# Performance work log

Hardware: AMD Instinct MI355X
Metric: run time of the kernel (lower is better)

## Reference

```python
import jax, jax.numpy as jnp
import numpy as np

B, P, E, H = 2, 4096, 512, 8
D = E // H
EPS = 1e-5


def _layernorm2d(x, g, b):
    # LayerNorm over last two dims (patches, embed) jointly, per torch nn.LayerNorm([P, E])
    mu = jnp.mean(x, axis=(-2, -1), keepdims=True)
    var = jnp.mean(jnp.square(x - mu), axis=(-2, -1), keepdims=True)
    return (x - mu) * jax.lax.rsqrt(var + EPS) * g + b


def setup_inputs() -> dict:
    key = jax.random.key(0)
    ks = jax.random.split(key, 4)
    s_in = 1.0 / np.sqrt(E)
    s_hid = 1.0 / np.sqrt(3 * E)
    return {
        "x": jax.random.normal(ks[0], (B, P, E), dtype=jnp.float32),
        "g1": jnp.ones((P, E), jnp.float32),
        "b1": jnp.zeros((P, E), jnp.float32),
        "W1": jax.random.normal(ks[1], (3 * E, E), jnp.float32) * s_in,
        "g2": jnp.ones((P, E), jnp.float32),
        "b2": jnp.zeros((P, E), jnp.float32),
        "Wa": jax.random.normal(ks[2], (3 * E, E), jnp.float32) * s_in,
        "ba": jnp.zeros((3 * E,), jnp.float32),
        "Wb": jax.random.normal(ks[3], (E, 3 * E), jnp.float32) * s_hid,
        "bb": jnp.zeros((E,), jnp.float32),
    }


def reference(x, g1, b1, W1, g2, b2, Wa, ba, Wb, bb):
    # --- attention branch ---
    h = _layernorm2d(x, g1, b1)                      # [B,P,E]
    qkv = h @ W1.T                                   # [B,P,3E]
    qkv = qkv.reshape(B, P, 3, H, D).transpose(2, 0, 3, 1, 4)  # [3,B,H,P,D]
    q, k, v = qkv[0], qkv[1], qkv[2]
    scale = 1.0 / jnp.sqrt(jnp.float32(D))
    dp = jnp.einsum("bhqd,bhkd->bhqk", q, k) * scale  # [B,H,P,P]
    # NOTE: softmax over axis -2 (the query axis), as in the original code
    dp = jax.nn.softmax(dp, axis=-2)
    wv = jnp.einsum("bhqk,bhkd->bhqd", dp, v)        # [B,H,P,D]
    wv = wv.transpose(0, 2, 1, 3).reshape(B, P, E)   # [B,P,E]
    out1 = x + wv
    # --- MLP branch ---
    h2 = _layernorm2d(out1, g2, b2)
    h2 = jax.nn.gelu(h2 @ Wa.T + ba, approximate=False)
    h2 = jax.nn.gelu(h2 @ Wb.T + bb, approximate=False)
    return h2 + out1
```

## Files before the change

### kernel.cpp

```cpp
#include <hip/hip_runtime.h>
#include <math.h>

typedef __bf16 bf16x8 __attribute__((ext_vector_type(8)));
typedef __bf16 bf16x4 __attribute__((ext_vector_type(4)));
typedef short s16x4 __attribute__((ext_vector_type(4)));
typedef float f32x4 __attribute__((ext_vector_type(4)));
typedef unsigned int u32x2 __attribute__((ext_vector_type(2)));
typedef unsigned short u16;
typedef unsigned int u32;

__device__ __forceinline__ void gl_lds16(const void* g, void* l) {
  __builtin_amdgcn_global_load_lds(
      (const __attribute__((address_space(1))) void*)g,
      (__attribute__((address_space(3))) void*)l, 16, 0, 0);
}

__device__ __forceinline__ u16 f2bf(float x) {
  union { float f; u32 u; } v; v.f = x;
  u32 r = v.u + 0x7FFFu + ((v.u >> 16) & 1u);
  return (u16)(r >> 16);
}

__device__ __forceinline__ u32 pack_bf2(float a, float b) {
  union { float f; u32 u; } ua, ub; ua.f = a; ub.f = b;
  return ((ua.u + 0x8000u) >> 16) | ((ub.u + 0x8000u) & 0xFFFF0000u);
}

__device__ __forceinline__ float expfast(float x) {
#if __has_builtin(__builtin_amdgcn_exp2f)
  return __builtin_amdgcn_exp2f(x);
#else
  return exp2f(x);
#endif
}

__device__ __forceinline__ f32x4 mfma16(bf16x4 a, bf16x4 b, f32x4 c) {
#if __has_builtin(__builtin_amdgcn_mfma_f32_16x16x16_bf16)
  return __builtin_amdgcn_mfma_f32_16x16x16_bf16(a, b, c, 0, 0, 0);
#else
  return __builtin_amdgcn_mfma_f32_16x16x16bf16_1k(
      __builtin_bit_cast(s16x4, a), __builtin_bit_cast(s16x4, b), c, 0, 0, 0);
#endif
}

__device__ __forceinline__ float gelu_f(float v) {
  return 0.5f * v * (1.0f + erff(v * 0.7071067811865475f));
}

__global__ void castbf3(const float* __restrict__ s0, const float* __restrict__ s1,
                        const float* __restrict__ s2, u16* __restrict__ d0,
                        u16* __restrict__ d1, u16* __restrict__ d2) {
  int blk = blockIdx.x;
  const float* s; u16* d;
  if (blk < 768)       { s = s0; d = d0; }
  else if (blk < 1536) { s = s1; d = d1; blk -= 768; }
  else                 { s = s2; d = d2; blk -= 1536; }
  int i = blk * 256 + threadIdx.x;
  float4 v = ((const float4*)s)[i];
  uint2 o;
  o.x = (u32)f2bf(v.x) | ((u32)f2bf(v.y) << 16);
  o.y = (u32)f2bf(v.z) | ((u32)f2bf(v.w) << 16);
  ((uint2*)d)[i] = o;
}

__global__ void ln_reduce(const float* __restrict__ src, float2* __restrict__ part) {
  int b = blockIdx.y;
  const float4* p = (const float4*)(src + (size_t)b * 2097152 + (size_t)blockIdx.x * 16384);
  float s = 0.f, q = 0.f;
  #pragma unroll
  for (int i = 0; i < 16; i++) {
    float4 v = p[i * 256 + threadIdx.x];
    s += v.x + v.y + v.z + v.w;
    q += v.x * v.x + v.y * v.y + v.z * v.z + v.w * v.w;
  }
  #pragma unroll
  for (int off = 32; off; off >>= 1) { s += __shfl_down(s, off, 64); q += __shfl_down(q, off, 64); }
  __shared__ float ls[4], lq[4];
  int w = threadIdx.x >> 6;
  if ((threadIdx.x & 63) == 0) { ls[w] = s; lq[w] = q; }
  __syncthreads();
  if (threadIdx.x == 0)
    part[b * 128 + blockIdx.x] =
        make_float2(ls[0] + ls[1] + ls[2] + ls[3], lq[0] + lq[1] + lq[2] + lq[3]);
}

__global__ void ln_final(const float2* __restrict__ part, float2* __restrict__ stats) {
  int b = blockIdx.x, t = threadIdx.x;
  float2 a = part[b * 128 + t], c = part[b * 128 + 64 + t];
  float s = a.x + c.x, q = a.y + c.y;
  #pragma unroll
  for (int off = 32; off; off >>= 1) { s += __shfl_down(s, off, 64); q += __shfl_down(q, off, 64); }
  if (t == 0) {
    const float inv = 1.0f / 2097152.0f;
    float mu = s * inv, var = q * inv - mu * mu;
    stats[b] = make_float2(mu, rsqrtf(var + 1e-5f));
  }
}

__global__ void ln_apply(const float* __restrict__ src, const float* __restrict__ g,
                         const float* __restrict__ bta, const float2* __restrict__ stats,
                         u16* __restrict__ dst) {
  int i = blockIdx.x * 256 + threadIdx.x;
  int b = i >= 524288;
  float2 st = stats[b];
  int r = i - b * 524288;
  float4 v = ((const float4*)src)[i];
  float4 gv = ((const float4*)g)[r];
  float4 bv = ((const float4*)bta)[r];
  float h0 = (v.x - st.x) * st.y * gv.x + bv.x;
  float h1 = (v.y - st.x) * st.y * gv.y + bv.y;
  float h2 = (v.z - st.x) * st.y * gv.z + bv.z;
  float h3 = (v.w - st.x) * st.y * gv.w + bv.w;
  uint2 o;
  o.x = (u32)f2bf(h0) | ((u32)f2bf(h1) << 16);
  o.y = (u32)f2bf(h2) | ((u32)f2bf(h3) << 16);
  ((uint2*)dst)[i] = o;
}

template <int MODE>
__global__ __launch_bounds__(256, 2)
void gemm_bt(const u16* __restrict__ A, const u16* __restrict__ Bm,
             const float* __restrict__ bias, const float* __restrict__ res,
             float* __restrict__ outf, u16* __restrict__ outb,
             int M, int N, int K) {
  __shared__ u16 As[128 * 32], Bs[128 * 32];
  const int tid = threadIdx.x;
  const int m0 = blockIdx.y * 128, n0 = blockIdx.x * 128;
  const int lane = tid & 63, w = tid >> 6;
  const int wm = (w >> 1) * 64, wn = (w & 1) * 64;
  const int c = lane & 15, quad = lane >> 4;
  const int arow = tid >> 2, acol = (tid & 3) * 8;

  const u16* gA = A + (size_t)(m0 + arow) * K + acol;
  const u16* gB = Bm + (size_t)(n0 + arow) * K + acol;
  u16* lA = As + tid * 8;
  u16* lB = Bs + tid * 8;

  f32x4 acc[4][4] = {};
  for (int kt = 0; kt < K; kt += 32) {
    gl_lds16(gA, lA);
    gl_lds16(gA + (size_t)64 * K, lA + 64 * 32);
    gl_lds16(gB, lB);
    gl_lds16(gB + (size_t)64 * K, lB + 64 * 32);
    gA += 32; gB += 32;
    __syncthreads();
    bf16x8 af[4], bf[4];
    #pragma unroll
    for (int i = 0; i < 4; i++) {
      af[i] = *(const bf16x8*)&As[(wm + i * 16 + c) * 32 + quad * 8];
      bf[i] = *(const bf16x8*)&Bs[(wn + i * 16 + c) * 32 + quad * 8];
    }
    #pragma unroll
    for (int i = 0; i < 4; i++)
      #pragma unroll
      for (int j = 0; j < 4; j++)
        acc[i][j] = __builtin_amdgcn_mfma_f32_16x16x32_bf16(af[i], bf[j], acc[i][j], 0, 0, 0);
    __syncthreads();
  }
  #pragma unroll
  for (int i = 0; i < 4; i++) {
    const int row0 = m0 + wm + i * 16 + quad * 4;
    #pragma unroll
    for (int j = 0; j < 4; j++) {
      const int col = n0 + wn + j * 16 + c;
      #pragma unroll
      for (int r = 0; r < 4; r++) {
        float v = acc[i][j][r];
        size_t oi = (size_t)(row0 + r) * N + col;
        if (MODE == 0 && col < 512) v *= 0.1803368801111204f;
        if (MODE == 1 || MODE == 2) v = gelu_f(v + bias[col]);
        if (MODE == 2) outf[oi] = v + res[oi];
        else           outb[oi] = f2bf(v);
      }
    }
  }
}

__global__ __launch_bounds__(256, 4)
void attn_pass1(const u16* __restrict__ qkv, float* __restrict__ rlpart) {
  __shared__ u16 Qs[2][2 * 128 * 32];
  const int tid = threadIdx.x;
  const int bh = blockIdx.y, b = bh >> 3, h = bh & 7;
  const int k0 = blockIdx.x * 128;
  const int lane = tid & 63, w = tid >> 6;
  const int wn = w * 32;
  const int c = lane & 15, quad = lane >> 4;
  const int arow = tid >> 2, acol = (tid & 3) * 8;

  bf16x8 bk[2][2];
  {
    const u16* Kg = qkv + ((size_t)(b * 4096 + k0 + wn + c)) * 1536 + 512 + h * 64 + quad * 8;
    #pragma unroll
    for (int j = 0; j < 2; j++)
      #pragma unroll
      for (int ks = 0; ks < 2; ks++)
        bk[j][ks] = *(const bf16x8*)(Kg + (size_t)j * 16 * 1536 + ks * 32);
  }
  const u16* Qg = qkv + ((size_t)(b * 4096 + blockIdx.z * 2048)) * 1536 + h * 64;

  #define STAGE_Q(t)                                                              \
    {                                                                             \
      u16* dst = Qs[(t) & 1];                                                     \
      const u16* src = Qg + (size_t)((t) * 128) * 1536;                           \
      _Pragma("unroll")                                                           \
      for (int ks = 0; ks < 2; ks++)                                              \
        _Pragma("unroll")                                                         \
        for (int rr = 0; rr < 128; rr += 64)                                      \
          gl_lds16(src + (size_t)(rr + arow) * 1536 + ks * 32 + acol,             \
                   dst + ks * 4096 + (rr + arow) * 32 + acol);                    \
    }

  STAGE_Q(0);
  float s0 = 0.f, s1 = 0.f;
  for (int t = 0; t < 16; t++) {
    __syncthreads();
    if (t + 1 < 16) STAGE_Q(t + 1);
    const u16* buf = Qs[t & 1];
    #pragma unroll
    for (int i = 0; i < 8; i++) {
      bf16x8 a0 = *(const bf16x8*)&buf[(i * 16 + c) * 32 + quad * 8];
      bf16x8 a1 = *(const bf16x8*)&buf[4096 + (i * 16 + c) * 32 + quad * 8];
      f32x4 acc0 = {}, acc1 = {};
      acc0 = __builtin_amdgcn_mfma_f32_16x16x32_bf16(a0, bk[0][0], acc0, 0, 0, 0);
      acc0 = __builtin_amdgcn_mfma_f32_16x16x32_bf16(a1, bk[0][1], acc0, 0, 0, 0);
      acc1 = __builtin_amdgcn_mfma_f32_16x16x32_bf16(a0, bk[1][0], acc1, 0, 0, 0);
      acc1 = __builtin_amdgcn_mfma_f32_16x16x32_bf16(a1, bk[1][1], acc1, 0, 0, 0);
      #pragma unroll
      for (int r = 0; r < 4; r++) {
        s0 += expfast(acc0[r]);
        s1 += expfast(acc1[r]);
      }
    }
  }
  #undef STAGE_Q
  s0 += __shfl_xor(s0, 16, 64); s0 += __shfl_xor(s0, 32, 64);
  s1 += __shfl_xor(s1, 16, 64); s1 += __shfl_xor(s1, 32, 64);
  if (quad == 0) {
    float* rp = rlpart + ((size_t)blockIdx.z * 16 + bh) * 4096 + k0 + wn;
    rp[c] = s0;
    rp[16 + c] = s1;
  }
}

__global__ void rl_comb(const float* __restrict__ part, float* __restrict__ rl) {
  int i = blockIdx.x * 256 + threadIdx.x;
  rl[i] = 1.0f / (part[i] + part[65536 + i]);
}

__global__ void vtrans(const u16* __restrict__ qkv, const float* __restrict__ rl,
                       u16* __restrict__ vt) {
  __shared__ u16 t[64 * 66];
  int bh = blockIdx.y, p0 = blockIdx.x * 64;
  int b = bh >> 3, h = bh & 7;
  const u16* src = qkv + ((size_t)(b * 4096 + p0)) * 1536 + 1024 + h * 64;
  const float* rp = rl + (size_t)bh * 4096 + p0;
  int tid = threadIdx.x;
  #pragma unroll
  for (int j = 0; j < 16; j++) {
    int idx = j * 256 + tid;
    int p = idx >> 6, d = idx & 63;
    union { float f; u32 u; } uv;
    uv.u = ((u32)src[(size_t)p * 1536 + d]) << 16;
    t[d * 66 + p] = f2bf(uv.f * rp[p]);
  }
  __syncthreads();
  u16* dst = vt + (size_t)bh * 262144 + (size_t)blockIdx.x * 4096;
  #pragma unroll
  for (int j = 0; j < 16; j++) {
    int idx = j * 256 + tid;
    int d = idx >> 6, p = idx & 63;
    dst[d * 64 + ((((p >> 3) & 7) ^ (d & 7)) << 3) + (p & 7)] = t[d * 66 + p];
  }
}

__global__ __launch_bounds__(256, 2)
void attn_pass2(const u16* __restrict__ qkv, const u16* __restrict__ vt,
                const float* __restrict__ x, float* __restrict__ out1) {
  __shared__ u16 Ks[2][2][2048];
  __shared__ u16 Vs[2][4096];
  const int tid = threadIdx.x;
  const int bh = blockIdx.y, b = bh >> 3, h = bh & 7;
  const int q0 = blockIdx.x * 128;
  const int lane = tid & 63, w = tid >> 6;
  const int wq = w * 32;
  const int c = lane & 15, quad = lane >> 4;

  bf16x8 bq[2][2];
  {
    const u16* Qg = qkv + ((size_t)(b * 4096 + q0 + wq + c)) * 1536 + h * 64 + quad * 8;
    #pragma unroll
    for (int j = 0; j < 2; j++)
      #pragma unroll
      for (int ks = 0; ks < 2; ks++)
        bq[j][ks] = *(const bf16x8*)(Qg + (size_t)j * 16 * 1536 + ks * 32);
  }
  const u16* Kg = qkv + ((size_t)b * 4096) * 1536 + 512 + h * 64;
  const u16* Vg = vt + (size_t)bh * 262144;

  #define STAGE_KV(t)                                                             \
    {                                                                             \
      const int buf_ = (t) & 1;                                                   \
      const int krow_ = (t) * 64 + (tid >> 2);                                    \
      _Pragma("unroll")                                                           \
      for (int ks = 0; ks < 2; ks++)                                              \
        gl_lds16(Kg + (size_t)krow_ * 1536 + ks * 32 + (tid & 3) * 8,             \
                 &Ks[buf_][ks][tid * 8]);                                         \
      gl_lds16(Vg + (t) * 4096 + tid * 8, &Vs[buf_][tid * 8]);                    \
      gl_lds16(Vg + (t) * 4096 + 2048 + tid * 8, &Vs[buf_][2048 + tid * 8]);      \
    }

  STAGE_KV(0);
  f32x4 oacc[2][4] = {};
  for (int t = 0; t < 64; t++) {
    __syncthreads();
    if (t + 1 < 64) STAGE_KV(t + 1);
    const int buf = t & 1;

    f32x4 sacc[4][2] = {};
    #pragma unroll
    for (int i = 0; i < 4; i++) {
      bf16x8 af0 = *(const bf16x8*)&Ks[buf][0][(i * 16 + c) * 32 + quad * 8];
      bf16x8 af1 = *(const bf16x8*)&Ks[buf][1][(i * 16 + c) * 32 + quad * 8];
      #pragma unroll
      for (int j = 0; j < 2; j++) {
        sacc[i][j] = __builtin_amdgcn_mfma_f32_16x16x32_bf16(af0, bq[j][0], sacc[i][j], 0, 0, 0);
        sacc[i][j] = __builtin_amdgcn_mfma_f32_16x16x32_bf16(af1, bq[j][1], sacc[i][j], 0, 0, 0);
      }
    }
    bf16x4 pa[4][2];
    #pragma unroll
    for (int i = 0; i < 4; i++)
      #pragma unroll
      for (int j = 0; j < 2; j++) {
        u32x2 pk;
        pk.x = pack_bf2(expfast(sacc[i][j][0]), expfast(sacc[i][j][1]));
        pk.y = pack_bf2(expfast(sacc[i][j][2]), expfast(sacc[i][j][3]));
        pa[i][j] = __builtin_bit_cast(bf16x4, pk);
      }
    #pragma unroll
    for (int kc = 0; kc < 4; kc++) {
      const int kb = 2 * kc + (quad >> 1);
      #pragma unroll
      for (int j2 = 0; j2 < 4; j2++) {
        const int d = j2 * 16 + c;
        bf16x4 vf = *(const bf16x4*)&Vs[buf][d * 64 + ((kb ^ (d & 7)) << 3) + 4 * (quad & 1)];
        oacc[0][j2] = mfma16(pa[kc][0], vf, oacc[0][j2]);
        oacc[1][j2] = mfma16(pa[kc][1], vf, oacc[1][j2]);
      }
    }
  }
  #undef STAGE_KV
  #pragma unroll
  for (int i2 = 0; i2 < 2; i2++)
    #pragma unroll
    for (int j2 = 0; j2 < 4; j2++)
      #pragma unroll
      for (int r = 0; r < 4; r++) {
        const int q = q0 + wq + i2 * 16 + quad * 4 + r;
        const int d = j2 * 16 + c;
        size_t oi = ((size_t)(b * 4096 + q)) * 512 + h * 64 + d;
        out1[oi] = x[oi] + oacc[i2][j2][r];
      }
}

extern "C" void kernel_launch(void* const* d_in, const int* in_sizes, int n_in,
                              void* d_out, int out_size, void* d_ws, size_t ws_size,
                              hipStream_t stream) {
  const float* x  = (const float*)d_in[0];
  const float* g1 = (const float*)d_in[1];
  const float* b1 = (const float*)d_in[2];
  const float* W1 = (const float*)d_in[3];
  const float* g2 = (const float*)d_in[4];
  const float* b2 = (const float*)d_in[5];
  const float* Wa = (const float*)d_in[6];
  const float* ba = (const float*)d_in[7];
  const float* Wb = (const float*)d_in[8];
  const float* bb = (const float*)d_in[9];
  float* out = (float*)d_out;

  char* ws = (char*)d_ws;
  u16* w1b   = (u16*)(ws);
  u16* wab   = (u16*)(ws + 1572864);
  u16* wbb   = (u16*)(ws + 3145728);
  u16* h1    = (u16*)(ws + 4718592);
  u16* qkv   = (u16*)(ws + 13107200);
  u16* vt    = (u16*)(ws + 38273024);
  u16* h2    = (u16*)(ws + 46661632);
  u16* mid   = (u16*)(ws + 55050240);
  float* rl  = (float*)(ws + 80216064);
  float* o1  = (float*)(ws + 80478208);
  float2* part  = (float2*)(ws + 97255424);
  float2* stats = (float2*)(ws + 97257472);
  float* rlpart = (float*)(ws + 55050240);

  castbf3<<<2304, 256, 0, stream>>>(W1, Wa, Wb, w1b, wab, wbb);

  ln_reduce<<<dim3(128, 2), 256, 0, stream>>>(x, part);
  ln_final<<<2, 64, 0, stream>>>(part, stats);
  ln_apply<<<4096, 256, 0, stream>>>(x, g1, b1, stats, h1);

  gemm_bt<0><<<dim3(12, 64), 256, 0, stream>>>(h1, w1b, nullptr, nullptr, nullptr, qkv,
                                               8192, 1536, 512);
  attn_pass1<<<dim3(32, 16, 2), 256, 0, stream>>>(qkv, rlpart);
  rl_comb<<<256, 256, 0, stream>>>(rlpart, rl);
  vtrans<<<dim3(64, 16), 256, 0, stream>>>(qkv, rl, vt);
  attn_pass2<<<dim3(32, 16), 256, 0, stream>>>(qkv, vt, x, o1);

  ln_reduce<<<dim3(128, 2), 256, 0, stream>>>(o1, part);
  ln_final<<<2, 64, 0, stream>>>(part, stats);
  ln_apply<<<4096, 256, 0, stream>>>(o1, g2, b2, stats, h2);

  gemm_bt<1><<<dim3(12, 64), 256, 0, stream>>>(h2, wab, ba, nullptr, nullptr, mid,
                                               8192, 1536, 512);
  gemm_bt<2><<<dim3(4, 64), 256, 0, stream>>>(mid, wbb, bb, o1, out, nullptr,
                                              8192, 512, 1536);
}
```

Before: 389.0 us.

## Fuse small launches and use 16x16x32 MFMA with LDS-staged probabilities in attention

Merges the weight casts with the first LayerNorm reduction into one launch. It also folds the LayerNorm finalization into each ln_apply block and the reciprocal-sum combine into vtrans, which removes four small kernel launches and their serialization. In attn_pass2, the exponentiated scores are written to a swizzled LDS buffer and read back as 8-wide fragments, so the PV product uses the 16x16x32 MFMA instead of 16x16x16. This trades extra LDS traffic and redundant per-block stat reductions for fewer launches and a denser MFMA instruction.

Result: faster. 367.3 us (-5.6%).

```diff
diff --git a/kernel.cpp b/kernel.cpp
--- a/kernel.cpp
+++ b/kernel.cpp
@@ -3,9 +3,7 @@
 
 typedef __bf16 bf16x8 __attribute__((ext_vector_type(8)));
 typedef __bf16 bf16x4 __attribute__((ext_vector_type(4)));
-typedef short s16x4 __attribute__((ext_vector_type(4)));
 typedef float f32x4 __attribute__((ext_vector_type(4)));
-typedef unsigned int u32x2 __attribute__((ext_vector_type(2)));
 typedef unsigned short u16;
 typedef unsigned int u32;
 
@@ -34,33 +32,47 @@
 #endif
 }
 
-__device__ __forceinline__ f32x4 mfma16(bf16x4 a, bf16x4 b, f32x4 c) {
-#if __has_builtin(__builtin_amdgcn_mfma_f32_16x16x16_bf16)
-  return __builtin_amdgcn_mfma_f32_16x16x16_bf16(a, b, c, 0, 0, 0);
-#else
-  return __builtin_amdgcn_mfma_f32_16x16x16bf16_1k(
-      __builtin_bit_cast(s16x4, a), __builtin_bit_cast(s16x4, b), c, 0, 0, 0);
-#endif
-}
-
 __device__ __forceinline__ float gelu_f(float v) {
   return 0.5f * v * (1.0f + erff(v * 0.7071067811865475f));
 }
 
-__global__ void castbf3(const float* __restrict__ s0, const float* __restrict__ s1,
-                        const float* __restrict__ s2, u16* __restrict__ d0,
-                        u16* __restrict__ d1, u16* __restrict__ d2) {
+__global__ void cast_lnred(const float* __restrict__ s0, const float* __restrict__ s1,
+                           const float* __restrict__ s2, u16* __restrict__ d0,
+                           u16* __restrict__ d1, u16* __restrict__ d2,
+                           const float* __restrict__ x, float2* __restrict__ part) {
   int blk = blockIdx.x;
-  const float* s; u16* d;
-  if (blk < 768)       { s = s0; d = d0; }
-  else if (blk < 1536) { s = s1; d = d1; blk -= 768; }
-  else                 { s = s2; d = d2; blk -= 1536; }
-  int i = blk * 256 + threadIdx.x;
-  float4 v = ((const float4*)s)[i];
-  uint2 o;
-  o.x = (u32)f2bf(v.x) | ((u32)f2bf(v.y) << 16);
-  o.y = (u32)f2bf(v.z) | ((u32)f2bf(v.w) << 16);
-  ((uint2*)d)[i] = o;
+  if (blk < 2304) {
+    const float* s; u16* d;
+    if (blk < 768)       { s = s0; d = d0; }
+    else if (blk < 1536) { s = s1; d = d1; blk -= 768; }
+    else                 { s = s2; d = d2; blk -= 1536; }
+    int i = blk * 256 + threadIdx.x;
+    float4 v = ((const float4*)s)[i];
+    uint2 o;
+    o.x = (u32)f2bf(v.x) | ((u32)f2bf(v.y) << 16);
+    o.y = (u32)f2bf(v.z) | ((u32)f2bf(v.w) << 16);
+    ((uint2*)d)[i] = o;
+    return;
+  }
+  blk -= 2304;
+  int b = blk >> 7, ib = blk & 127;
+  const float4* p = (const float4*)(x + (size_t)b * 2097152 + (size_t)ib * 16384);
+  float s = 0.f, q = 0.f;
+  #pragma unroll
+  for (int i = 0; i < 16; i++) {
+    float4 v = p[i * 256 + threadIdx.x];
+    s += v.x + v.y + v.z + v.w;
+    q += v.x * v.x + v.y * v.y + v.z * v.z + v.w * v.w;
+  }
+  #pragma unroll
+  for (int off = 32; off; off >>= 1) { s += __shfl_down(s, off, 64); q += __shfl_down(q, off, 64); }
+  __shared__ float ls[4], lq[4];
+  int w = threadIdx.x >> 6;
+  if ((threadIdx.x & 63) == 0) { ls[w] = s; lq[w] = q; }
+  __syncthreads();
+  if (threadIdx.x == 0)
+    part[b * 128 + ib] =
+        make_float2(ls[0] + ls[1] + ls[2] + ls[3], lq[0] + lq[1] + lq[2] + lq[3]);
 }
 
 __global__ void ln_reduce(const float* __restrict__ src, float2* __restrict__ part) {
@@ -84,33 +96,28 @@
         make_float2(ls[0] + ls[1] + ls[2] + ls[3], lq[0] + lq[1] + lq[2] + lq[3]);
 }
 
-__global__ void ln_final(const float2* __restrict__ part, float2* __restrict__ stats) {
-  int b = blockIdx.x, t = threadIdx.x;
-  float2 a = part[b * 128 + t], c = part[b * 128 + 64 + t];
-  float s = a.x + c.x, q = a.y + c.y;
-  #pragma unroll
-  for (int off = 32; off; off >>= 1) { s += __shfl_down(s, off, 64); q += __shfl_down(q, off, 64); }
-  if (t == 0) {
-    const float inv = 1.0f / 2097152.0f;
-    float mu = s * inv, var = q * inv - mu * mu;
-    stats[b] = make_float2(mu, rsqrtf(var + 1e-5f));
-  }
-}
-
 __global__ void ln_apply(const float* __restrict__ src, const float* __restrict__ g,
-                         const float* __restrict__ bta, const float2* __restrict__ stats,
+                         const float* __restrict__ bta, const float2* __restrict__ part,
                          u16* __restrict__ dst) {
   int i = blockIdx.x * 256 + threadIdx.x;
   int b = i >= 524288;
-  float2 st = stats[b];
+  int lane = threadIdx.x & 63;
+  float2 a = part[b * 128 + lane], c2 = part[b * 128 + 64 + lane];
+  float s = a.x + c2.x, q = a.y + c2.y;
+  #pragma unroll
+  for (int off = 32; off; off >>= 1) { s += __shfl_down(s, off, 64); q += __shfl_down(q, off, 64); }
+  s = __shfl(s, 0, 64); q = __shfl(q, 0, 64);
+  const float inv = 1.0f / 2097152.0f;
+  float mu = s * inv;
+  float rsig = rsqrtf(q * inv - mu * mu + 1e-5f);
   int r = i - b * 524288;
   float4 v = ((const float4*)src)[i];
   float4 gv = ((const float4*)g)[r];
   float4 bv = ((const float4*)bta)[r];
-  float h0 = (v.x - st.x) * st.y * gv.x + bv.x;
-  float h1 = (v.y - st.x) * st.y * gv.y + bv.y;
-  float h2 = (v.z - st.x) * st.y * gv.z + bv.z;
-  float h3 = (v.w - st.x) * st.y * gv.w + bv.w;
+  float h0 = (v.x - mu) * rsig * gv.x + bv.x;
+  float h1 = (v.y - mu) * rsig * gv.y + bv.y;
+  float h2 = (v.z - mu) * rsig * gv.z + bv.z;
+  float h3 = (v.w - mu) * rsig * gv.w + bv.w;
   uint2 o;
   o.x = (u32)f2bf(h0) | ((u32)f2bf(h1) << 16);
   o.y = (u32)f2bf(h2) | ((u32)f2bf(h3) << 16);
@@ -242,26 +249,26 @@
   }
 }
 
-__global__ void rl_comb(const float* __restrict__ part, float* __restrict__ rl) {
-  int i = blockIdx.x * 256 + threadIdx.x;
-  rl[i] = 1.0f / (part[i] + part[65536 + i]);
-}
-
-__global__ void vtrans(const u16* __restrict__ qkv, const float* __restrict__ rl,
+__global__ void vtrans(const u16* __restrict__ qkv, const float* __restrict__ rlpart,
                        u16* __restrict__ vt) {
   __shared__ u16 t[64 * 66];
+  __shared__ float rls[64];
   int bh = blockIdx.y, p0 = blockIdx.x * 64;
   int b = bh >> 3, h = bh & 7;
   const u16* src = qkv + ((size_t)(b * 4096 + p0)) * 1536 + 1024 + h * 64;
-  const float* rp = rl + (size_t)bh * 4096 + p0;
   int tid = threadIdx.x;
+  if (tid < 64) {
+    size_t idx = (size_t)bh * 4096 + p0 + tid;
+    rls[tid] = 1.0f / (rlpart[idx] + rlpart[65536 + idx]);
+  }
+  __syncthreads();
   #pragma unroll
   for (int j = 0; j < 16; j++) {
     int idx = j * 256 + tid;
     int p = idx >> 6, d = idx & 63;
     union { float f; u32 u; } uv;
     uv.u = ((u32)src[(size_t)p * 1536 + d]) << 16;
-    t[d * 66 + p] = f2bf(uv.f * rp[p]);
+    t[d * 66 + p] = f2bf(uv.f * rls[p]);
   }
   __syncthreads();
   u16* dst = vt + (size_t)bh * 262144 + (size_t)blockIdx.x * 4096;
@@ -278,6 +285,7 @@
                 const float* __restrict__ x, float* __restrict__ out1) {
   __shared__ u16 Ks[2][2][2048];
   __shared__ u16 Vs[2][4096];
+  __shared__ u16 Ps[128][64];
   const int tid = threadIdx.x;
   const int bh = blockIdx.y, b = bh >> 3, h = bh & 7;
   const int q0 = blockIdx.x * 128;
@@ -327,39 +335,52 @@
         sacc[i][j] = __builtin_amdgcn_mfma_f32_16x16x32_bf16(af1, bq[j][1], sacc[i][j], 0, 0, 0);
       }
     }
-    bf16x4 pa[4][2];
-    #pragma unroll
-    for (int i = 0; i < 4; i++)
+    #pragma unroll
+    for (int i = 0; i < 4; i++) {
+      const int blk = i * 2 + (quad >> 1);
       #pragma unroll
       for (int j = 0; j < 2; j++) {
-        u32x2 pk;
+        const int qloc = wq + j * 16 + c;
+        u16* pp = &Ps[qloc][((blk ^ (qloc & 7)) << 3) + ((quad & 1) << 2)];
+        uint2 pk;
         pk.x = pack_bf2(expfast(sacc[i][j][0]), expfast(sacc[i][j][1]));
         pk.y = pack_bf2(expfast(sacc[i][j][2]), expfast(sacc[i][j][3]));
-        pa[i][j] = __builtin_bit_cast(bf16x4, pk);
-      }
-    #pragma unroll
-    for (int kc = 0; kc < 4; kc++) {
-      const int kb = 2 * kc + (quad >> 1);
-      #pragma unroll
-      for (int j2 = 0; j2 < 4; j2++) {
-        const int d = j2 * 16 + c;
-        bf16x4 vf = *(const bf16x4*)&Vs[buf][d * 64 + ((kb ^ (d & 7)) << 3) + 4 * (quad & 1)];
-        oacc[0][j2] = mfma16(pa[kc][0], vf, oacc[0][j2]);
-        oacc[1][j2] = mfma16(pa[kc][1], vf, oacc[1][j2]);
-      }
+        *(uint2*)pp = pk;
+      }
+    }
+    #pragma unroll
+    for (int kg = 0; kg < 2; kg++) {
+      bf16x8 pf[2], vf[4];
+      #pragma unroll
+      for (int j = 0; j < 2; j++) {
+        const int qloc = wq + j * 16 + c;
+        const int blk = kg * 4 + quad;
+        pf[j] = *(const bf16x8*)&Ps[qloc][(blk ^ (qloc & 7)) << 3];
+      }
+      #pragma unroll
+      for (int dt = 0; dt < 4; dt++) {
+        const int d = dt * 16 + c;
+        const int vblk = kg * 4 + quad;
+        vf[dt] = *(const bf16x8*)&Vs[buf][d * 64 + ((vblk ^ (d & 7)) << 3)];
+      }
+      #pragma unroll
+      for (int j = 0; j < 2; j++)
+        #pragma unroll
+        for (int dt = 0; dt < 4; dt++)
+          oacc[j][dt] = __builtin_amdgcn_mfma_f32_16x16x32_bf16(pf[j], vf[dt], oacc[j][dt], 0, 0, 0);
     }
   }
   #undef STAGE_KV
   #pragma unroll
-  for (int i2 = 0; i2 < 2; i2++)
-    #pragma unroll
-    for (int j2 = 0; j2 < 4; j2++)
+  for (int j = 0; j < 2; j++)
+    #pragma unroll
+    for (int dt = 0; dt < 4; dt++)
       #pragma unroll
       for (int r = 0; r < 4; r++) {
-        const int q = q0 + wq + i2 * 16 + quad * 4 + r;
-        const int d = j2 * 16 + c;
+        const int q = q0 + wq + j * 16 + quad * 4 + r;
+        const int d = dt * 16 + c;
         size_t oi = ((size_t)(b * 4096 + q)) * 512 + h * 64 + d;
-        out1[oi] = x[oi] + oacc[i2][j2][r];
+        out1[oi] = x[oi] + oacc[j][dt][r];
       }
 }
 
@@ -387,28 +408,21 @@
   u16* vt    = (u16*)(ws + 38273024);
   u16* h2    = (u16*)(ws + 46661632);
   u16* mid   = (u16*)(ws + 55050240);
-  float* rl  = (float*)(ws + 80216064);
   float* o1  = (float*)(ws + 80478208);
   float2* part  = (float2*)(ws + 97255424);
-  float2* stats = (float2*)(ws + 97257472);
   float* rlpart = (float*)(ws + 55050240);
 
-  castbf3<<<2304, 256, 0, stream>>>(W1, Wa, Wb, w1b, wab, wbb);
-
-  ln_reduce<<<dim3(128, 2), 256, 0, stream>>>(x, part);
-  ln_final<<<2, 64, 0, stream>>>(part, stats);
-  ln_apply<<<4096, 256, 0, stream>>>(x, g1, b1, stats, h1);
+  cast_lnred<<<2560, 256, 0, stream>>>(W1, Wa, Wb, w1b, wab, wbb, x, part);
+  ln_apply<<<4096, 256, 0, stream>>>(x, g1, b1, part, h1);
 
   gemm_bt<0><<<dim3(12, 64), 256, 0, stream>>>(h1, w1b, nullptr, nullptr, nullptr, qkv,
                                                8192, 1536, 512);
   attn_pass1<<<dim3(32, 16, 2), 256, 0, stream>>>(qkv, rlpart);
-  rl_comb<<<256, 256, 0, stream>>>(rlpart, rl);
-  vtrans<<<dim3(64, 16), 256, 0, stream>>>(qkv, rl, vt);
+  vtrans<<<dim3(64, 16), 256, 0, stream>>>(qkv, rlpart, vt);
   attn_pass2<<<dim3(32, 16), 256, 0, stream>>>(qkv, vt, x, o1);
 
   ln_reduce<<<dim3(128, 2), 256, 0, stream>>>(o1, part);
-  ln_final<<<2, 64, 0, stream>>>(part, stats);
-  ln_apply<<<4096, 256, 0, stream>>>(o1, g2, b2, stats, h2);
+  ln_apply<<<4096, 256, 0, stream>>>(o1, g2, b2, part, h2);
 
   gemm_bt<1><<<dim3(12, 64), 256, 0, stream>>>(h2, wab, ba, nullptr, nullptr, mid,
                                                8192, 1536, 512);
```
